# Kernel tuning notes

Hardware: AMD Instinct MI355X
Metric: run time of the kernel (lower is better)

Reference implementation:

```python
import jax, jax.numpy as jnp
import numpy as np

NUM_TASKS = 50
NUM_EXPERTS = 8
WIDTH = 1024
FEAT = 512
HEAD_DIM = 256
BATCH = 4096


def setup_inputs() -> dict:
    key = jax.random.key(0)
    ks = jax.random.split(key, 8)
    feats = jax.random.normal(ks[0], (BATCH, FEAT), jnp.float32)
    tids = jax.random.randint(ks[1], (BATCH,), 0, NUM_TASKS)
    onehot = jax.nn.one_hot(tids, NUM_TASKS, dtype=jnp.float32)
    x = jnp.concatenate([feats, onehot], axis=-1)  # [B, FEAT + NUM_TASKS]

    def he(k, shape, fan_in):
        return jax.random.normal(k, shape, jnp.float32) * np.float32(np.sqrt(2.0 / fan_in))

    W_emb = he(ks[2], (NUM_TASKS, NUM_EXPERTS), NUM_TASKS)
    b_emb = jnp.zeros((NUM_EXPERTS,), jnp.float32)
    # expert MLP: depth=2 hidden layers + output layer, vmapped over experts
    W0 = he(ks[3], (NUM_EXPERTS, FEAT, WIDTH), FEAT)
    b0 = jnp.zeros((NUM_EXPERTS, WIDTH), jnp.float32)
    W1 = he(ks[4], (NUM_EXPERTS, WIDTH, WIDTH), WIDTH)
    b1 = jnp.zeros((NUM_EXPERTS, WIDTH), jnp.float32)
    Wout = he(ks[5], (NUM_EXPERTS, WIDTH, WIDTH), WIDTH)
    bout = jnp.zeros((NUM_EXPERTS, WIDTH), jnp.float32)
    # per-task heads
    W_head = he(ks[6], (NUM_TASKS, WIDTH, HEAD_DIM), WIDTH)
    b_head = jnp.zeros((NUM_TASKS, HEAD_DIM), jnp.float32)
    return {"x": x, "W_emb": W_emb, "b_emb": b_emb, "W0": W0, "b0": b0,
            "W1": W1, "b1": b1, "Wout": Wout, "bout": bout,
            "W_head": W_head, "b_head": b_head}


def _gram_schmidt(x):
    # x: [B, E, D]; classical Gram-Schmidt over expert axis (sequential recurrence)
    basis = x[:, :1, :] / jnp.linalg.norm(x[:, :1, :], axis=-1, keepdims=True)
    for i in range(1, x.shape[1]):
        v = x[:, i:i + 1, :]                                   # [B,1,D]
        coeff = jnp.einsum('bij,bkj->bik', v, basis)           # [B,1,k]
        w = v - jnp.einsum('bik,bkd->bid', coeff, basis)       # [B,1,D]
        w = w / jnp.linalg.norm(w, axis=-1, keepdims=True)
        basis = jnp.concatenate((basis, w), axis=1)
    return basis  # [B,E,D]


def reference(x, W_emb, b_emb, W0, b0, W1, b1, Wout, bout, W_head, b_head):
    task_idx = x[:, -NUM_TASKS:]                 # one-hot [B,T]
    feat = x[:, :-NUM_TASKS]                     # [B,F]
    emb = task_idx @ W_emb + b_emb               # [B,E]
    h = jax.nn.relu(jnp.einsum('bf,efw->bew', feat, W0) + b0)   # [B,E,W]
    h = jax.nn.relu(jnp.einsum('bew,ewk->bek', h, W1) + b1)
    experts_out = jnp.einsum('bew,ewk->bek', h, Wout) + bout    # [B,E,W]
    experts_out = _gram_schmidt(experts_out)
    feats_out = jax.nn.relu(jnp.einsum('bek,be->bk', experts_out, emb))  # [B,W]
    heads = jnp.einsum('bk,tkd->btd', feats_out, W_head) + b_head        # [B,T,H]
    tids = jnp.argmax(task_idx, axis=-1)
    return heads[jnp.arange(x.shape[0]), tids]   # [B,H]
```

## Files before the change

kernel.cpp:

```cpp
#include <hip/hip_runtime.h>
#include <hip/hip_bf16.h>

#define NUM_TASKS 50
#define NUM_EXPERTS 8
#define WIDTH 1024
#define FEAT 512
#define HEAD_DIM 256
#define BATCH 4096
#define XCOLS (FEAT + NUM_TASKS)

typedef unsigned short ushort_t;
typedef short bf16x8 __attribute__((ext_vector_type(8)));
typedef float f32x4 __attribute__((ext_vector_type(4)));

__device__ __forceinline__ ushort_t f2b(float f) {
    unsigned u = __float_as_uint(f);
    unsigned r = (u + 0x7fffu + ((u >> 16) & 1u)) >> 16;
    return (ushort_t)r;
}
__device__ __forceinline__ float b2f_lo(unsigned u) { return __uint_as_float(u << 16); }
__device__ __forceinline__ float b2f_hi(unsigned u) { return __uint_as_float(u & 0xffff0000u); }

__device__ __forceinline__ void async16(const ushort_t* g, ushort_t* l) {
    __builtin_amdgcn_global_load_lds(
        (const __attribute__((address_space(1))) unsigned int*)g,
        (__attribute__((address_space(3))) unsigned int*)l,
        16, 0, 0);
}

__global__ void prep_kernel(const float* __restrict__ x,
                            const float* __restrict__ W_emb,
                            const float* __restrict__ b_emb,
                            float* __restrict__ emb,
                            int* __restrict__ tids) {
    int b = blockIdx.x;
    int lane = threadIdx.x;
    float v = 0.f;
    if (lane < NUM_TASKS) v = x[(size_t)b * XCOLS + FEAT + lane];
    unsigned long long mask = __ballot(v > 0.5f);
    int tid = __ffsll(mask) - 1;
    if (tid < 0) tid = 0;
    if (tid > NUM_TASKS - 1) tid = NUM_TASKS - 1;
    if (lane == 0) tids[b] = tid;
    if (lane < NUM_EXPERTS)
        emb[(size_t)b * NUM_EXPERTS + lane] =
            W_emb[tid * NUM_EXPERTS + lane] + b_emb[lane];
}

__global__ void sort_kernel(const int* __restrict__ tids,
                            int* __restrict__ pos,
                            int* __restrict__ row_map,
                            int* __restrict__ tstart,
                            int* __restrict__ tcnt) {
    __shared__ int cnt[NUM_TASKS];
    __shared__ int start[NUM_TASKS];
    __shared__ int rank[NUM_TASKS];
    int t = threadIdx.x;
    if (t < NUM_TASKS) { cnt[t] = 0; rank[t] = 0; }
    __syncthreads();
    for (int b = t; b < BATCH; b += 256) atomicAdd(&cnt[tids[b]], 1);
    __syncthreads();
    if (t == 0) {
        int acc = 0;
        for (int k = 0; k < NUM_TASKS; ++k) { start[k] = acc; acc += cnt[k]; }
    }
    __syncthreads();
    if (t < NUM_TASKS) { tstart[t] = start[t]; tcnt[t] = cnt[t]; }
    for (int b = t; b < BATCH; b += 256) {
        int tk = tids[b];
        int p = start[tk] + atomicAdd(&rank[tk], 1);
        pos[b] = p;
        row_map[p] = b;
    }
}

__global__ void conv_x_kernel(const float* __restrict__ x, ushort_t* __restrict__ xb) {
    int b = blockIdx.x, t = threadIdx.x;
    #pragma unroll
    for (int q = 0; q < 2; ++q) {
        int i = t + 256 * q;
        xb[(size_t)b * FEAT + i] = f2b(x[(size_t)b * XCOLS + i]);
    }
}

__global__ void conv_t_kernel(const float* __restrict__ src, ushort_t* __restrict__ dst,
                              int R, int C) {
    int r0 = blockIdx.x * 32, c0 = blockIdx.y * 32, z = blockIdx.z;
    __shared__ float tile[32][33];
    const float* S = src + (size_t)z * R * C;
    ushort_t* D = dst + (size_t)z * R * C;
    int t = threadIdx.x;
    #pragma unroll
    for (int q = 0; q < 4; ++q) {
        int i = t + 256 * q; int ri = i >> 5, ci = i & 31;
        tile[ri][ci] = S[(size_t)(r0 + ri) * C + c0 + ci];
    }
    __syncthreads();
    #pragma unroll
    for (int q = 0; q < 4; ++q) {
        int i = t + 256 * q; int ci = i >> 5, ri = i & 31;
        D[(size_t)(c0 + ci) * R + r0 + ri] = f2b(tile[ri][ci]);
    }
}

template <bool RELU>
__global__ __launch_bounds__(256) void mfma_gemm(
    const ushort_t* __restrict__ A, int lda, int aoff,
    const ushort_t* __restrict__ Bt,
    const float* __restrict__ bias,
    ushort_t* __restrict__ C, int K)
{
    const int m0 = blockIdx.x * 128;
    const int n0 = blockIdx.y * 128;
    const int e  = blockIdx.z;
    const int t  = threadIdx.x;
    const int l  = t & 63;

    __shared__ __align__(16) ushort_t As[128 * 64];
    __shared__ __align__(16) ushort_t Bs[128 * 64];

    const ushort_t* __restrict__ Ab = A + (size_t)e * aoff + (size_t)m0 * lda;
    const ushort_t* __restrict__ Bb = Bt + ((size_t)e * WIDTH + n0) * K;

    const int sr = t >> 3;
    const int sk = ((t & 7) ^ (sr & 7)) * 8;

    const int w  = t >> 6;
    const int wm = (w >> 1) * 64;
    const int wn = (w & 1) * 64;
    const int lm = l & 15;
    const int lq = l >> 4;
    const int ss = lm & 7;

    f32x4 acc[4][4];
    #pragma unroll
    for (int i = 0; i < 4; ++i)
        #pragma unroll
        for (int j = 0; j < 4; ++j) acc[i][j] = {0.f, 0.f, 0.f, 0.f};

    for (int kt = 0; kt < K; kt += 64) {
        __syncthreads();
        #pragma unroll
        for (int p = 0; p < 4; ++p) {
            async16(Ab + (size_t)(p * 32 + sr) * lda + kt + sk, &As[p * 2048 + t * 8]);
            async16(Bb + (size_t)(p * 32 + sr) * K   + kt + sk, &Bs[p * 2048 + t * 8]);
        }
        __syncthreads();

        #pragma unroll
        for (int ks = 0; ks < 2; ++ks) {
            const int slot = ((ks * 4 + lq) ^ ss) * 8;
            bf16x8 af[4], bfr[4];
            #pragma unroll
            for (int mi = 0; mi < 4; ++mi)
                af[mi] = *reinterpret_cast<const bf16x8*>(&As[(wm + mi * 16 + lm) * 64 + slot]);
            #pragma unroll
            for (int ni = 0; ni < 4; ++ni)
                bfr[ni] = *reinterpret_cast<const bf16x8*>(&Bs[(wn + ni * 16 + lm) * 64 + slot]);
            #pragma unroll
            for (int mi = 0; mi < 4; ++mi)
                #pragma unroll
                for (int ni = 0; ni < 4; ++ni)
                    acc[mi][ni] = __builtin_amdgcn_mfma_f32_16x16x32_bf16(
                        af[mi], bfr[ni], acc[mi][ni], 0, 0, 0);
        }
    }

    const int rbase = lq * 4;
    #pragma unroll
    for (int mi = 0; mi < 4; ++mi) {
        #pragma unroll
        for (int ni = 0; ni < 4; ++ni) {
            int col = n0 + wn + ni * 16 + lm;
            float bv = bias[e * WIDTH + col];
            #pragma unroll
            for (int r = 0; r < 4; ++r) {
                int row = m0 + wm + mi * 16 + rbase + r;
                float v = acc[mi][ni][r] + bv;
                if (RELU) v = fmaxf(v, 0.f);
                C[(size_t)row * (NUM_EXPERTS * WIDTH) + e * WIDTH + col] = f2b(v);
            }
        }
    }
}

__device__ __forceinline__ float wave_sum(float x) {
    #pragma unroll
    for (int off = 1; off < 64; off <<= 1) x += __shfl_xor(x, off, 64);
    return x;
}
__device__ __forceinline__ void u2f8(uint4 a, float* f) {
    f[0] = b2f_lo(a.x); f[1] = b2f_hi(a.x);
    f[2] = b2f_lo(a.y); f[3] = b2f_hi(a.y);
    f[4] = b2f_lo(a.z); f[5] = b2f_hi(a.z);
    f[6] = b2f_lo(a.w); f[7] = b2f_hi(a.w);
}

__global__ __launch_bounds__(256, 1) void gs_wave_kernel(
    const ushort_t* __restrict__ eo,
    const float* __restrict__ emb,
    const int* __restrict__ pos,
    ushort_t* __restrict__ featsB)
{
    const int w = threadIdx.x >> 6;
    const int l = threadIdx.x & 63;
    const int r = blockIdx.x * 4 + w;

    float v[NUM_EXPERTS][16];
    const ushort_t* row = eo + (size_t)r * (NUM_EXPERTS * WIDTH);
    #pragma unroll
    for (int e = 0; e < NUM_EXPERTS; ++e) {
        const uint4* p = reinterpret_cast<const uint4*>(row + e * WIDTH + l * 16);
        u2f8(p[0], &v[e][0]);
        u2f8(p[1], &v[e][8]);
    }

    {
        float s = 0.f;
        #pragma unroll
        for (int j = 0; j < 16; ++j) s += v[0][j] * v[0][j];
        s = wave_sum(s);
        float inv = 1.f / sqrtf(s);
        #pragma unroll
        for (int j = 0; j < 16; ++j) v[0][j] *= inv;
    }

    #pragma unroll
    for (int i = 1; i < NUM_EXPERTS; ++i) {
        float c[NUM_EXPERTS];
        #pragma unroll
        for (int jj = 0; jj < i; ++jj) {
            float p = 0.f;
            #pragma unroll
            for (int j = 0; j < 16; ++j) p += v[i][j] * v[jj][j];
            c[jj] = wave_sum(p);
        }
        float s = 0.f;
        #pragma unroll
        for (int j = 0; j < 16; ++j) {
            float wv = v[i][j];
            #pragma unroll
            for (int jj = 0; jj < i; ++jj) wv -= c[jj] * v[jj][j];
            v[i][j] = wv;
            s += wv * wv;
        }
        s = wave_sum(s);
        float inv = 1.f / sqrtf(s);
        #pragma unroll
        for (int j = 0; j < 16; ++j) v[i][j] *= inv;
    }

    float er[NUM_EXPERTS];
    #pragma unroll
    for (int e = 0; e < NUM_EXPERTS; ++e) er[e] = emb[(size_t)r * NUM_EXPERTS + e];
    float f[16];
    #pragma unroll
    for (int j = 0; j < 16; ++j) {
        float s = 0.f;
        #pragma unroll
        for (int e = 0; e < NUM_EXPERTS; ++e) s += v[e][j] * er[e];
        f[j] = fmaxf(s, 0.f);
    }
    unsigned u[8];
    #pragma unroll
    for (int j = 0; j < 8; ++j)
        u[j] = (unsigned)f2b(f[2 * j]) | ((unsigned)f2b(f[2 * j + 1]) << 16);
    int p = pos[r];
    uint4* dst = reinterpret_cast<uint4*>(featsB + (size_t)p * WIDTH + l * 16);
    dst[0] = make_uint4(u[0], u[1], u[2], u[3]);
    dst[1] = make_uint4(u[4], u[5], u[6], u[7]);
}

__global__ __launch_bounds__(256) void head_mfma(
    const ushort_t* __restrict__ featsB,
    const int* __restrict__ row_map,
    const int* __restrict__ tstart,
    const int* __restrict__ tcnt,
    const ushort_t* __restrict__ Wht,
    const float* __restrict__ b_head,
    float* __restrict__ out)
{
    const int task = blockIdx.y;
    const int mt   = blockIdx.x;
    const int cnt  = tcnt[task];
    if (mt * 32 >= cnt) return;
    const int ts = tstart[task];
    const int t = threadIdx.x;
    const int l = t & 63;
    const int w = t >> 6;

    __shared__ __align__(16) ushort_t As[32 * 64];
    __shared__ __align__(16) ushort_t Bs[256 * 64];

    const int sr = t >> 3;
    const int sk = ((t & 7) ^ (sr & 7)) * 8;

    const int lm = l & 15;
    const int lq = l >> 4;
    const int ss = lm & 7;

    int arow = ts + mt * 32 + sr;
    if (arow > BATCH - 1) arow = BATCH - 1;
    const ushort_t* __restrict__ Asrc = featsB + (size_t)arow * WIDTH;
    const ushort_t* __restrict__ Bsrc = Wht + (size_t)task * HEAD_DIM * WIDTH;

    f32x4 acc[2][4];
    #pragma unroll
    for (int i = 0; i < 2; ++i)
        #pragma unroll
        for (int j = 0; j < 4; ++j) acc[i][j] = {0.f, 0.f, 0.f, 0.f};

    for (int kt = 0; kt < WIDTH; kt += 64) {
        __syncthreads();
        async16(Asrc + kt + sk, &As[t * 8]);
        #pragma unroll
        for (int p = 0; p < 8; ++p) {
            int n = p * 32 + sr;
            async16(Bsrc + (size_t)n * WIDTH + kt + sk, &Bs[p * 2048 + t * 8]);
        }
        __syncthreads();

        #pragma unroll
        for (int ks = 0; ks < 2; ++ks) {
            const int slot = ((ks * 4 + lq) ^ ss) * 8;
            bf16x8 af[2], bfr[4];
            #pragma unroll
            for (int mi = 0; mi < 2; ++mi)
                af[mi] = *reinterpret_cast<const bf16x8*>(&As[(mi * 16 + lm) * 64 + slot]);
            #pragma unroll
            for (int ni = 0; ni < 4; ++ni)
                bfr[ni] = *reinterpret_cast<const bf16x8*>(&Bs[(w * 64 + ni * 16 + lm) * 64 + slot]);
            #pragma unroll
            for (int mi = 0; mi < 2; ++mi)
                #pragma unroll
                for (int ni = 0; ni < 4; ++ni)
                    acc[mi][ni] = __builtin_amdgcn_mfma_f32_16x16x32_bf16(
                        af[mi], bfr[ni], acc[mi][ni], 0, 0, 0);
        }
    }

    const int rbase = lq * 4;
    #pragma unroll
    for (int ni = 0; ni < 4; ++ni) {
        int d = w * 64 + ni * 16 + lm;
        float bhv = b_head[task * HEAD_DIM + d];
        #pragma unroll
        for (int mi = 0; mi < 2; ++mi) {
            #pragma unroll
            for (int r = 0; r < 4; ++r) {
                int mrow = mt * 32 + mi * 16 + rbase + r;
                if (mrow < cnt) {
                    int b = row_map[ts + mrow];
                    out[(size_t)b * HEAD_DIM + d] = acc[mi][ni][r] + bhv;
                }
            }
        }
    }
}

extern "C" void kernel_launch(void* const* d_in, const int* in_sizes, int n_in,
                              void* d_out, int out_size, void* d_ws, size_t ws_size,
                              hipStream_t stream) {
    const float* x      = (const float*)d_in[0];
    const float* W_emb  = (const float*)d_in[1];
    const float* b_emb  = (const float*)d_in[2];
    const float* W0     = (const float*)d_in[3];
    const float* b0     = (const float*)d_in[4];
    const float* W1     = (const float*)d_in[5];
    const float* b1     = (const float*)d_in[6];
    const float* Wout   = (const float*)d_in[7];
    const float* bout   = (const float*)d_in[8];
    const float* W_head = (const float*)d_in[9];
    const float* b_head = (const float*)d_in[10];
    float* out = (float*)d_out;

    char* ws = (char*)d_ws;
    size_t off = 0;
    auto take = [&](size_t bytes) { char* p = ws + off; off += (bytes + 255) & ~(size_t)255; return p; };
    float*    emb     = (float*)   take((size_t)BATCH * NUM_EXPERTS * sizeof(float));
    int*      tids    = (int*)     take((size_t)BATCH * sizeof(int));
    int*      pos     = (int*)     take((size_t)BATCH * sizeof(int));
    int*      row_map = (int*)     take((size_t)BATCH * sizeof(int));
    int*      tstart  = (int*)     take((size_t)NUM_TASKS * sizeof(int));
    int*      tcnt    = (int*)     take((size_t)NUM_TASKS * sizeof(int));
    ushort_t* xb      = (ushort_t*)take((size_t)BATCH * FEAT * 2);
    ushort_t* W0t     = (ushort_t*)take((size_t)NUM_EXPERTS * WIDTH * FEAT * 2);
    ushort_t* W1t     = (ushort_t*)take((size_t)NUM_EXPERTS * WIDTH * WIDTH * 2);
    ushort_t* Woutt   = (ushort_t*)take((size_t)NUM_EXPERTS * WIDTH * WIDTH * 2);
    ushort_t* Wht     = (ushort_t*)take((size_t)NUM_TASKS * HEAD_DIM * WIDTH * 2);
    ushort_t* featsB  = (ushort_t*)take((size_t)BATCH * WIDTH * 2);
    char* bufbase = ws + off;

    const size_t ROWB = (size_t)NUM_EXPERTS * WIDTH * 2;
    size_t avail = ws_size > off ? ws_size - off : 0;
    int CHUNK;
    if      (avail >= 2 * (size_t)4096 * ROWB) CHUNK = 4096;
    else if (avail >= 2 * (size_t)2048 * ROWB) CHUNK = 2048;
    else if (avail >= 2 * (size_t)1024 * ROWB) CHUNK = 1024;
    else                                       CHUNK = 512;

    ushort_t* bufA = (ushort_t*)bufbase;
    ushort_t* bufB = (ushort_t*)(bufbase + (size_t)CHUNK * ROWB);

    prep_kernel<<<BATCH, 64, 0, stream>>>(x, W_emb, b_emb, emb, tids);
    sort_kernel<<<1, 256, 0, stream>>>(tids, pos, row_map, tstart, tcnt);
    conv_x_kernel<<<BATCH, 256, 0, stream>>>(x, xb);
    conv_t_kernel<<<dim3(FEAT / 32, WIDTH / 32, NUM_EXPERTS), 256, 0, stream>>>(W0, W0t, FEAT, WIDTH);
    conv_t_kernel<<<dim3(WIDTH / 32, WIDTH / 32, NUM_EXPERTS), 256, 0, stream>>>(W1, W1t, WIDTH, WIDTH);
    conv_t_kernel<<<dim3(WIDTH / 32, WIDTH / 32, NUM_EXPERTS), 256, 0, stream>>>(Wout, Woutt, WIDTH, WIDTH);
    conv_t_kernel<<<dim3(WIDTH / 32, HEAD_DIM / 32, NUM_TASKS), 256, 0, stream>>>(W_head, Wht, WIDTH, HEAD_DIM);

    dim3 grid(CHUNK / 128, WIDTH / 128, NUM_EXPERTS);
    for (int r0 = 0; r0 < BATCH; r0 += CHUNK) {
        const ushort_t* xc = xb + (size_t)r0 * FEAT;
        mfma_gemm<true ><<<grid, 256, 0, stream>>>(xc, FEAT, 0, W0t, b0, bufA, FEAT);
        mfma_gemm<true ><<<grid, 256, 0, stream>>>(bufA, NUM_EXPERTS * WIDTH, WIDTH, W1t, b1, bufB, WIDTH);
        mfma_gemm<false><<<grid, 256, 0, stream>>>(bufB, NUM_EXPERTS * WIDTH, WIDTH, Woutt, bout, bufA, WIDTH);
        gs_wave_kernel<<<CHUNK / 4, 256, 0, stream>>>(bufA, emb + (size_t)r0 * NUM_EXPERTS,
                                                      pos + r0, featsB);
    }
    head_mfma<<<dim3(6, NUM_TASKS), 256, 0, stream>>>(featsB, row_map, tstart, tcnt,
                                                      Wht, b_head, out);
}
```

Before: 487.7 us.

## Use 32x32 MFMA in expert GEMM, vectorize weight transpose, fuse x conversion

The expert GEMM switches from 16x16x32 to 32x32x16 bf16 MFMA, with 2x2 accumulator tiles per wave, so fewer LDS fragment reads are issued per flop. The weight transpose/convert kernel moves to 64x64 tiles with float4 loads and packed bf16 pair stores, replacing scalar accesses. The feature-to-bf16 conversion is folded into the prep kernel as vectorized per-lane stores, removing one launch. The epilogue row mapping changes to match the 32x32 output layout, which is a correctness risk if the layout assumption is wrong.

```diff
diff --git a/kernel.cpp b/kernel.cpp
--- a/kernel.cpp
+++ b/kernel.cpp
@@ -12,6 +12,7 @@
 typedef unsigned short ushort_t;
 typedef short bf16x8 __attribute__((ext_vector_type(8)));
 typedef float f32x4 __attribute__((ext_vector_type(4)));
+typedef float f32x16 __attribute__((ext_vector_type(16)));
 
 __device__ __forceinline__ ushort_t f2b(float f) {
     unsigned u = __float_as_uint(f);
@@ -28,15 +29,17 @@
         16, 0, 0);
 }
 
-__global__ void prep_kernel(const float* __restrict__ x,
-                            const float* __restrict__ W_emb,
-                            const float* __restrict__ b_emb,
-                            float* __restrict__ emb,
-                            int* __restrict__ tids) {
+__global__ void prepx_kernel(const float* __restrict__ x,
+                             const float* __restrict__ W_emb,
+                             const float* __restrict__ b_emb,
+                             float* __restrict__ emb,
+                             int* __restrict__ tids,
+                             ushort_t* __restrict__ xb) {
     int b = blockIdx.x;
     int lane = threadIdx.x;
+    const float* xr = x + (size_t)b * XCOLS;
     float v = 0.f;
-    if (lane < NUM_TASKS) v = x[(size_t)b * XCOLS + FEAT + lane];
+    if (lane < NUM_TASKS) v = xr[FEAT + lane];
     unsigned long long mask = __ballot(v > 0.5f);
     int tid = __ffsll(mask) - 1;
     if (tid < 0) tid = 0;
@@ -45,6 +48,15 @@
     if (lane < NUM_EXPERTS)
         emb[(size_t)b * NUM_EXPERTS + lane] =
             W_emb[tid * NUM_EXPERTS + lane] + b_emb[lane];
+    float f[8];
+    #pragma unroll
+    for (int j = 0; j < 8; ++j) f[j] = xr[lane * 8 + j];
+    unsigned u[4];
+    #pragma unroll
+    for (int j = 0; j < 4; ++j)
+        u[j] = (unsigned)f2b(f[2 * j]) | ((unsigned)f2b(f[2 * j + 1]) << 16);
+    *reinterpret_cast<uint4*>(xb + (size_t)b * FEAT + lane * 8) =
+        make_uint4(u[0], u[1], u[2], u[3]);
 }
 
 __global__ void sort_kernel(const int* __restrict__ tids,
@@ -74,32 +86,33 @@
     }
 }
 
-__global__ void conv_x_kernel(const float* __restrict__ x, ushort_t* __restrict__ xb) {
-    int b = blockIdx.x, t = threadIdx.x;
-    #pragma unroll
-    for (int q = 0; q < 2; ++q) {
-        int i = t + 256 * q;
-        xb[(size_t)b * FEAT + i] = f2b(x[(size_t)b * XCOLS + i]);
-    }
-}
-
-__global__ void conv_t_kernel(const float* __restrict__ src, ushort_t* __restrict__ dst,
-                              int R, int C) {
-    int r0 = blockIdx.x * 32, c0 = blockIdx.y * 32, z = blockIdx.z;
-    __shared__ float tile[32][33];
+__global__ __launch_bounds__(256) void conv_t64(const float* __restrict__ src,
+                                                ushort_t* __restrict__ dst,
+                                                int R, int C) {
+    int r0 = blockIdx.x * 64, c0 = blockIdx.y * 64, z = blockIdx.z;
+    __shared__ float tile[64][65];
     const float* S = src + (size_t)z * R * C;
     ushort_t* D = dst + (size_t)z * R * C;
     int t = threadIdx.x;
-    #pragma unroll
-    for (int q = 0; q < 4; ++q) {
-        int i = t + 256 * q; int ri = i >> 5, ci = i & 31;
-        tile[ri][ci] = S[(size_t)(r0 + ri) * C + c0 + ci];
+    const int ci4 = t & 15, ri = t >> 4;
+    #pragma unroll
+    for (int p = 0; p < 4; ++p) {
+        int r = ri + 16 * p;
+        float4 v = *reinterpret_cast<const float4*>(S + (size_t)(r0 + r) * C + c0 + ci4 * 4);
+        tile[r][ci4 * 4 + 0] = v.x;
+        tile[r][ci4 * 4 + 1] = v.y;
+        tile[r][ci4 * 4 + 2] = v.z;
+        tile[r][ci4 * 4 + 3] = v.w;
     }
     __syncthreads();
-    #pragma unroll
-    for (int q = 0; q < 4; ++q) {
-        int i = t + 256 * q; int ci = i >> 5, ri = i & 31;
-        D[(size_t)(c0 + ci) * R + r0 + ri] = f2b(tile[ri][ci]);
+    const int co2 = t & 31, ci = t >> 5;
+    #pragma unroll
+    for (int p = 0; p < 8; ++p) {
+        int c = ci + 8 * p;
+        float a = tile[co2 * 2 + 0][c];
+        float b = tile[co2 * 2 + 1][c];
+        unsigned u = (unsigned)f2b(a) | ((unsigned)f2b(b) << 16);
+        *reinterpret_cast<unsigned*>(D + (size_t)(c0 + c) * R + r0 + co2 * 2) = u;
     }
 }
 
@@ -128,15 +141,17 @@
     const int w  = t >> 6;
     const int wm = (w >> 1) * 64;
     const int wn = (w & 1) * 64;
-    const int lm = l & 15;
-    const int lq = l >> 4;
-    const int ss = lm & 7;
-
-    f32x4 acc[4][4];
-    #pragma unroll
-    for (int i = 0; i < 4; ++i)
-        #pragma unroll
-        for (int j = 0; j < 4; ++j) acc[i][j] = {0.f, 0.f, 0.f, 0.f};
+    const int ra = l & 31;
+    const int hi = l >> 5;
+    const int sx = l & 7;
+
+    f32x16 acc[2][2];
+    #pragma unroll
+    for (int i = 0; i < 2; ++i)
+        #pragma unroll
+        for (int j = 0; j < 2; ++j)
+            #pragma unroll
+            for (int q = 0; q < 16; ++q) acc[i][j][q] = 0.f;
 
     for (int kt = 0; kt < K; kt += 64) {
         __syncthreads();
@@ -148,34 +163,34 @@
         __syncthreads();
 
         #pragma unroll
-        for (int ks = 0; ks < 2; ++ks) {
-            const int slot = ((ks * 4 + lq) ^ ss) * 8;
-            bf16x8 af[4], bfr[4];
-            #pragma unroll
-            for (int mi = 0; mi < 4; ++mi)
-                af[mi] = *reinterpret_cast<const bf16x8*>(&As[(wm + mi * 16 + lm) * 64 + slot]);
-            #pragma unroll
-            for (int ni = 0; ni < 4; ++ni)
-                bfr[ni] = *reinterpret_cast<const bf16x8*>(&Bs[(wn + ni * 16 + lm) * 64 + slot]);
-            #pragma unroll
-            for (int mi = 0; mi < 4; ++mi)
+        for (int ks = 0; ks < 4; ++ks) {
+            const int slot = ((ks * 2 + hi) ^ sx) * 8;
+            bf16x8 af[2], bfr[2];
+            #pragma unroll
+            for (int mi = 0; mi < 2; ++mi)
+                af[mi] = *reinterpret_cast<const bf16x8*>(&As[(wm + mi * 32 + ra) * 64 + slot]);
+            #pragma unroll
+            for (int ni = 0; ni < 2; ++ni)
+                bfr[ni] = *reinterpret_cast<const bf16x8*>(&Bs[(wn + ni * 32 + ra) * 64 + slot]);
+            #pragma unroll
+            for (int mi = 0; mi < 2; ++mi)
                 #pragma unroll
-                for (int ni = 0; ni < 4; ++ni)
-                    acc[mi][ni] = __builtin_amdgcn_mfma_f32_16x16x32_bf16(
+                for (int ni = 0; ni < 2; ++ni)
+                    acc[mi][ni] = __builtin_amdgcn_mfma_f32_32x32x16_bf16(
                         af[mi], bfr[ni], acc[mi][ni], 0, 0, 0);
         }
     }
 
-    const int rbase = lq * 4;
-    #pragma unroll
-    for (int mi = 0; mi < 4; ++mi) {
-        #pragma unroll
-        for (int ni = 0; ni < 4; ++ni) {
-            int col = n0 + wn + ni * 16 + lm;
+    const int lrow = 4 * hi;
+    #pragma unroll
+    for (int mi = 0; mi < 2; ++mi) {
+        #pragma unroll
+        for (int ni = 0; ni < 2; ++ni) {
+            int col = n0 + wn + ni * 32 + ra;
             float bv = bias[e * WIDTH + col];
             #pragma unroll
-            for (int r = 0; r < 4; ++r) {
-                int row = m0 + wm + mi * 16 + rbase + r;
+            for (int r = 0; r < 16; ++r) {
+                int row = m0 + wm + mi * 32 + 8 * (r >> 2) + lrow + (r & 3);
                 float v = acc[mi][ni][r] + bv;
                 if (RELU) v = fmaxf(v, 0.f);
                 C[(size_t)row * (NUM_EXPERTS * WIDTH) + e * WIDTH + col] = f2b(v);
@@ -402,13 +417,12 @@
     ushort_t* bufA = (ushort_t*)bufbase;
     ushort_t* bufB = (ushort_t*)(bufbase + (size_t)CHUNK * ROWB);
 
-    prep_kernel<<<BATCH, 64, 0, stream>>>(x, W_emb, b_emb, emb, tids);
+    prepx_kernel<<<BATCH, 64, 0, stream>>>(x, W_emb, b_emb, emb, tids, xb);
     sort_kernel<<<1, 256, 0, stream>>>(tids, pos, row_map, tstart, tcnt);
-    conv_x_kernel<<<BATCH, 256, 0, stream>>>(x, xb);
-    conv_t_kernel<<<dim3(FEAT / 32, WIDTH / 32, NUM_EXPERTS), 256, 0, stream>>>(W0, W0t, FEAT, WIDTH);
-    conv_t_kernel<<<dim3(WIDTH / 32, WIDTH / 32, NUM_EXPERTS), 256, 0, stream>>>(W1, W1t, WIDTH, WIDTH);
-    conv_t_kernel<<<dim3(WIDTH / 32, WIDTH / 32, NUM_EXPERTS), 256, 0, stream>>>(Wout, Woutt, WIDTH, WIDTH);
-    conv_t_kernel<<<dim3(WIDTH / 32, HEAD_DIM / 32, NUM_TASKS), 256, 0, stream>>>(W_head, Wht, WIDTH, HEAD_DIM);
+    conv_t64<<<dim3(FEAT / 64, WIDTH / 64, NUM_EXPERTS), 256, 0, stream>>>(W0, W0t, FEAT, WIDTH);
+    conv_t64<<<dim3(WIDTH / 64, WIDTH / 64, NUM_EXPERTS), 256, 0, stream>>>(W1, W1t, WIDTH, WIDTH);
+    conv_t64<<<dim3(WIDTH / 64, WIDTH / 64, NUM_EXPERTS), 256, 0, stream>>>(Wout, Woutt, WIDTH, WIDTH);
+    conv_t64<<<dim3(WIDTH / 64, HEAD_DIM / 64, NUM_TASKS), 256, 0, stream>>>(W_head, Wht, WIDTH, HEAD_DIM);
 
     dim3 grid(CHUNK / 128, WIDTH / 128, NUM_EXPERTS);
     for (int r0 = 0; r0 < BATCH; r0 += CHUNK) {
```

Measured after the change: 460.8 us. 5.5% less time.
